# Kernel optimization log

Measured on AMD Instinct MI355X. Metric: run time of the kernel, lower is better.

The kernel has to match this reference:

```python
import jax, jax.numpy as jnp
import numpy as np

ALPHA = 0.2  # LeakyReLU negative slope
N, H, W, T, V = 4, 24, 24, 4, 32
L, NHEADS = 2, 4  # n_heads_per_layer = (4, 4)


def _norm_adj(Bp):
    # adj = B + I, min-max normalized, then symmetric D^-1/2 normalization
    v = Bp.shape[0]
    adj = Bp + jnp.eye(v, dtype=Bp.dtype)
    adj = (adj - adj.min()) / (adj.max() - adj.min())
    d12 = 1.0 / jnp.sqrt(jnp.sum(adj, axis=1))  # diag of sqrt(inverse(D))
    return d12[:, None] * adj * d12[None, :]


def _head(x, mw, mb, a, Bp):
    # x: (N,H,W,T,V) -> h: (N,V,H,W,T)
    n, hh, ww, tt, vv = x.shape
    h = jnp.transpose(x, (0, 4, 1, 2, 3))
    # LinearMapping over the T axis (in_features == out_features == T)
    Wh = jnp.einsum('nvhwt,ts->nvhws', h, mw) + mb  # (N,V,H,W,T)
    # temporal all-pairs attention input: concat on the W axis, then the
    # same C-order reinterpretation torch .view does:
    rep_i = jnp.repeat(Wh, vv, axis=1)            # (N,V*V,H,W,T), i-major
    rep_j = jnp.tile(Wh, (1, vv, 1, 1, 1))        # (N,V*V,H,W,T), j-major
    a_in = jnp.concatenate([rep_i, rep_j], axis=3)  # (N,V*V,H,2W,T)
    a_in = a_in.reshape(n, vv, vv, tt, 2 * hh * ww)  # == torch .view
    e = jnp.einsum('nijtk,k->nijt', a_in, a)
    att = jax.nn.softmax(jax.nn.leaky_relu(e, ALPHA), axis=-1)  # softmax over T
    # diag_embed + matmul over j == elementwise scale over t, summed over j
    Whf = Wh.reshape(n, vv, hh * ww, tt)
    agg = jnp.einsum('njmt,nijt->nimt', Whf, att)  # (N,V,HW,T)
    adjn = _norm_adj(Bp)
    hp = jnp.einsum('nimt,iu->nmtu', agg, adjn)    # (N,HW,T,V)
    return jax.nn.elu(hp.reshape(n, hh, ww, tt, vv))


def setup_inputs() -> dict:
    key = jax.random.key(0)
    k0, k1, k2, k3 = jax.random.split(key, 4)
    x = jax.random.normal(k0, (N, H, W, T, V), dtype=jnp.float32)
    # per-layer, per-head parameters
    map_w = jax.random.normal(k1, (L, NHEADS, T, T), dtype=jnp.float32) * 0.5
    map_b = jax.random.normal(k2, (L, NHEADS, T), dtype=jnp.float32) * 0.02
    # a_temporal: (2*H*W,) per head, xavier-ish scale
    a_temp = jax.random.normal(k3, (L, NHEADS, 2 * H * W), dtype=jnp.float32) * 0.05
    B_param = jnp.full((L, NHEADS, V, V), 1e-6, dtype=jnp.float32)
    return {"x": x, "map_w": map_w, "map_b": map_b, "a_temp": a_temp, "B_param": B_param}


def reference(x, map_w, map_b, a_temp, B_param):
    out = x
    for l in range(map_w.shape[0]):
        xi = out
        heads = jax.vmap(lambda mw, mb, a, Bp: _head(xi, mw, mb, a, Bp))(
            map_w[l], map_b[l], a_temp[l], B_param[l])
        out = jnp.mean(heads, axis=0)
    return out
```

## Files before the change

kernel.cpp:

```cpp
#include <hip/hip_runtime.h>

#define MM 576
#define NBLK 256
#define NTHR 512

__device__ __forceinline__ float lrelu(float x) { return x > 0.f ? x : 0.2f * x; }
__device__ __forceinline__ float elu1(float x)  { return x > 0.f ? x : (__expf(x) - 1.f); }
__device__ __forceinline__ unsigned short f2bf(float f) {
    unsigned u = __float_as_uint(f);
    return (unsigned short)((u + 0x7FFFu + ((u >> 16) & 1u)) >> 16);
}

__device__ __forceinline__ void wh_e_body(int n, int t, int s, int b,
                                          const float* __restrict__ xb,
                                          float* __restrict__ red,
                                          const float* __restrict__ mw_l,
                                          const float* __restrict__ mb_l,
                                          const float* __restrict__ a_l,
                                          unsigned short* __restrict__ Whg,
                                          float* __restrict__ ep) {
    int tid = threadIdx.x;
    int sub = tid >> 5, v = tid & 31;
    int hd = sub & 3, r0 = sub >> 2;
    unsigned short* Wb = Whg + (size_t)b * 4608;
    float ei = 0.f, ej = 0.f;
    for (int r = r0; r < 9; r += 4) {
        int rr = s * 9 + r;
        int dh = rr / 24, wc = rr % 24;
        const float* ab = a_l + hd * 1152 + dh * 192 + wc * 4;
        float4 aiv = *(const float4*)ab;
        float4 ajv = *(const float4*)(ab + 96);
        float x0 = xb[r * 128 + v],      x1 = xb[r * 128 + 32 + v];
        float x2 = xb[r * 128 + 64 + v], x3 = xb[r * 128 + 96 + v];
#pragma unroll
        for (int tt = 0; tt < 4; ++tt) {
            float wh = fmaf(x0, mw_l[hd * 16 + tt],
                        fmaf(x1, mw_l[hd * 16 + 4 + tt],
                         fmaf(x2, mw_l[hd * 16 + 8 + tt],
                          fmaf(x3, mw_l[hd * 16 + 12 + tt], mb_l[hd * 4 + tt]))));
            Wb[((hd * 4 + tt) * 9 + r) * 32 + v] = f2bf(wh);
            ei = fmaf(wh, (&aiv.x)[tt], ei);
            ej = fmaf(wh, (&ajv.x)[tt], ej);
        }
    }
    red[(sub * 2 + 0) * 32 + v] = ei;
    red[(sub * 2 + 1) * 32 + v] = ej;
    __syncthreads();
    if (tid < 256) {
        int hdx = tid >> 6, whx = (tid >> 5) & 1, vx = tid & 31;
        float e = 0.f;
#pragma unroll
        for (int k = 0; k < 4; ++k)
            e += red[((hdx + 4 * k) * 2 + whx) * 32 + vx];
        ep[(((size_t)(n * 4 + t)) * 16 + s) * 256 + tid] = e;
    }
}

__global__ __launch_bounds__(NTHR) void k1(const float* __restrict__ x,
                                           const float* __restrict__ map_w,
                                           const float* __restrict__ map_b,
                                           const float* __restrict__ a_temp,
                                           unsigned short* __restrict__ Whg,
                                           float* __restrict__ ep0) {
    __shared__ float xb[1152];
    __shared__ float red[1024];
    int b = blockIdx.x, tid = threadIdx.x;
    int n = b >> 6, t = (b >> 4) & 3, s = b & 15;
    if (tid < 288)
        ((float4*)xb)[tid] =
            ((const float4*)(x + (size_t)(n * MM + t * 144 + s * 9) * 128))[tid];
    __syncthreads();
    wh_e_body(n, t, s, b, xb, red, map_w, map_b, a_temp, Whg, ep0);
}

__device__ __forceinline__ void adj_build_one(const float* __restrict__ B,
                                              float* __restrict__ adjf,
                                              float* __restrict__ d12s) {
    int lane = threadIdx.x & 63;
    int u = lane & 31;
    float val[16], lmin = 1e30f, lmax = -1e30f;
#pragma unroll
    for (int k = 0; k < 16; ++k) {
        int p = lane + 64 * k;
        float vv = B[p] + ((p >> 5) == (p & 31) ? 1.f : 0.f);
        val[k] = vv;
        lmin = fminf(lmin, vv);
        lmax = fmaxf(lmax, vv);
    }
#pragma unroll
    for (int off = 32; off; off >>= 1) {
        lmin = fminf(lmin, __shfl_xor(lmin, off, 64));
        lmax = fmaxf(lmax, __shfl_xor(lmax, off, 64));
    }
    float inv = 1.f / (lmax - lmin);
    float d12r[16];
    int h = lane >> 5;
#pragma unroll
    for (int k = 0; k < 16; ++k) {
        float r = val[k];
#pragma unroll
        for (int off = 16; off; off >>= 1) r += __shfl_xor(r, off, 64);
        float rsn = (r - 32.f * lmin) * inv;
        d12r[k] = rsqrtf(rsn);
        if (u == 2 * k + h) d12s[u] = d12r[k];
    }
#pragma unroll
    for (int k = 0; k < 16; ++k) {
        int p = lane + 64 * k;
        adjf[p] = (val[k] - lmin) * inv * d12r[k] * d12s[p & 31];
    }
}

__global__ __launch_bounds__(256) void kC(const float* __restrict__ Bp_l,
                                          const float* __restrict__ ep,
                                          float* __restrict__ CT) {
    __shared__ float e[4][2][32];
    __shared__ float adjf[1024];
    __shared__ float attT[32 * 33];
    __shared__ float d12s[32];
    int b = blockIdx.x, tid = threadIdx.x;
    int n = b >> 4, hd = (b >> 2) & 3, q = b & 3;

    {
        int qp = tid >> 6, rest = tid & 63;
        const float* src = ep + ((size_t)(n * 4 + qp) * 16) * 256 + hd * 64 + rest;
        float a = 0.f;
#pragma unroll
        for (int ss = 0; ss < 16; ++ss) a += src[ss * 256];
        e[qp][rest >> 5][rest & 31] = a;
    }
    if (tid < 64) adj_build_one(Bp_l + (size_t)hd * 1024, adjf, d12s);
    __syncthreads();

    {
        int i = tid & 31;
        float ei0 = e[0][0][i], ei1 = e[1][0][i], ei2 = e[2][0][i], ei3 = e[3][0][i];
#pragma unroll
        for (int k = 0; k < 4; ++k) {
            int j = (tid + 256 * k) >> 5;
            float eq0 = lrelu(ei0 + e[0][1][j]);
            float eq1 = lrelu(ei1 + e[1][1][j]);
            float eq2 = lrelu(ei2 + e[2][1][j]);
            float eq3 = lrelu(ei3 + e[3][1][j]);
            float mx = fmaxf(fmaxf(eq0, eq1), fmaxf(eq2, eq3));
            eq0 = __expf(eq0 - mx); eq1 = __expf(eq1 - mx);
            eq2 = __expf(eq2 - mx); eq3 = __expf(eq3 - mx);
            float invs = __builtin_amdgcn_rcpf(eq0 + eq1 + eq2 + eq3);
            float num = (q & 2) ? ((q & 1) ? eq3 : eq2) : ((q & 1) ? eq1 : eq0);
            attT[j * 33 + i] = num * invs;
        }
    }
    __syncthreads();

    {
        int u = tid >> 3, j4 = (tid & 7) * 4;
        float c0 = 0.f, c1 = 0.f, c2 = 0.f, c3 = 0.f;
#pragma unroll
        for (int i = 0; i < 32; ++i) {
            float ad = adjf[i * 32 + u];
            c0 = fmaf(attT[(j4 + 0) * 33 + i], ad, c0);
            c1 = fmaf(attT[(j4 + 1) * 33 + i], ad, c1);
            c2 = fmaf(attT[(j4 + 2) * 33 + i], ad, c2);
            c3 = fmaf(attT[(j4 + 3) * 33 + i], ad, c3);
        }
        float4 cv = make_float4(c0, c1, c2, c3);
        *(float4*)&CT[(((size_t)(n * 4 + hd) * 4 + q) * 32 + u) * 32 + j4] = cv;
    }
}

template<bool LAST>
__device__ __forceinline__ void kG_body(const float* __restrict__ CT,
                                        unsigned short* __restrict__ Whg,
                                        const float* __restrict__ mw2,
                                        const float* __restrict__ mb2,
                                        const float* __restrict__ a2,
                                        float* __restrict__ ep_out,
                                        float* __restrict__ outg) {
    __shared__ unsigned short Whh[4][4][9][32];
    __shared__ float uf[3584];
    int b = blockIdx.x, tid = threadIdx.x;
    int n = b >> 6, t = (b >> 4) & 3, s = b & 15;
    int w = tid >> 6, lane = tid & 63;
    int g = w >> 2, tout = w & 3;
    int u = lane & 31, h = lane >> 5;

    float cc0[32], cc1[32];
    const float4* ct0 = (const float4*)(CT + (((size_t)(n * 4 + 2 * g) * 4 + tout) * 32 + u) * 32);
    const float4* ct1 = (const float4*)(CT + (((size_t)(n * 4 + 2 * g + 1) * 4 + tout) * 32 + u) * 32);
#pragma unroll
    for (int k = 0; k < 8; ++k) *(float4*)&cc0[4 * k] = ct0[k];
    {
        const unsigned* src = (const unsigned*)(Whg + (size_t)b * 4608);
        unsigned* dst = (unsigned*)&Whh[0][0][0][0];
#pragma unroll
        for (int k = 0; k < 4; ++k) dst[tid + 512 * k] = src[tid + 512 * k];
        if (tid < 256) dst[tid + 2048] = src[tid + 2048];
    }
#pragma unroll
    for (int k = 0; k < 8; ++k) *(float4*)&cc1[4 * k] = ct1[k];
    __syncthreads();

    float acc[5] = {0.f, 0.f, 0.f, 0.f, 0.f};
    auto gemm_hd = [&](int hd, const float (&cc)[32]) {
#pragma unroll
        for (int k = 0; k < 5; ++k) {
            int r = h ? (k < 4 ? 5 + k : 8) : k;
            const uint4* wr = (const uint4*)&Whh[hd][tout][r][0];
            float d = 0.f;
#pragma unroll
            for (int q4 = 0; q4 < 4; ++q4) {
                uint4 pk = wr[q4];
                d = fmaf(__uint_as_float(pk.x << 16),         cc[8 * q4 + 0], d);
                d = fmaf(__uint_as_float(pk.x & 0xFFFF0000u), cc[8 * q4 + 1], d);
                d = fmaf(__uint_as_float(pk.y << 16),         cc[8 * q4 + 2], d);
                d = fmaf(__uint_as_float(pk.y & 0xFFFF0000u), cc[8 * q4 + 3], d);
                d = fmaf(__uint_as_float(pk.z << 16),         cc[8 * q4 + 4], d);
                d = fmaf(__uint_as_float(pk.z & 0xFFFF0000u), cc[8 * q4 + 5], d);
                d = fmaf(__uint_as_float(pk.w << 16),         cc[8 * q4 + 6], d);
                d = fmaf(__uint_as_float(pk.w & 0xFFFF0000u), cc[8 * q4 + 7], d);
            }
            acc[k] += elu1(d);
        }
    };
    gemm_hd(2 * g,     cc0);
    gemm_hd(2 * g + 1, cc1);

    if (g == 1) {
        float* part = uf + 2304 + tout * 320;
#pragma unroll
        for (int k = 0; k < 5; ++k)
            if (h == 0 || k < 4) part[k * 64 + lane] = acc[k];
    }
    __syncthreads();
    if (g == 0) {
        const float* part = uf + 2304 + tout * 320;
#pragma unroll
        for (int k = 0; k < 5; ++k)
            if (h == 0 || k < 4) acc[k] += part[k * 64 + lane];
        if (LAST) {
            size_t mb = (size_t)(n * MM + t * 144 + s * 9);
#pragma unroll
            for (int k = 0; k < 5; ++k) {
                if (h == 0 || k < 4) {
                    int r = h ? 5 + k : k;
                    outg[((mb + r) * 4 + tout) * 32 + u] = 0.25f * acc[k];
                }
            }
        } else {
            float* xb = uf;
#pragma unroll
            for (int k = 0; k < 5; ++k) {
                if (h == 0 || k < 4) {
                    int r = h ? 5 + k : k;
                    xb[r * 128 + tout * 32 + u] = 0.25f * acc[k];
                }
            }
        }
    }

    if (!LAST) {
        __syncthreads();
        wh_e_body(n, t, s, b, uf, uf + 1216, mw2, mb2, a2, Whg, ep_out);
    }
}

__global__ __launch_bounds__(NTHR) void kG0(const float* __restrict__ CT,
                                            unsigned short* __restrict__ Whg,
                                            const float* __restrict__ mw2,
                                            const float* __restrict__ mb2,
                                            const float* __restrict__ a2,
                                            float* __restrict__ ep1) {
    kG_body<false>(CT, Whg, mw2, mb2, a2, ep1, nullptr);
}

__global__ __launch_bounds__(NTHR) void kG1(const float* __restrict__ CT,
                                            unsigned short* __restrict__ Whg,
                                            float* __restrict__ outg) {
    kG_body<true>(CT, Whg, nullptr, nullptr, nullptr, nullptr, outg);
}

extern "C" void kernel_launch(void* const* d_in, const int* in_sizes, int n_in,
                              void* d_out, int out_size, void* d_ws, size_t ws_size,
                              hipStream_t stream) {
    const float* x      = (const float*)d_in[0];
    const float* map_w  = (const float*)d_in[1];
    const float* map_b  = (const float*)d_in[2];
    const float* a_temp = (const float*)d_in[3];
    const float* Bp     = (const float*)d_in[4];
    float* out = (float*)d_out;

    unsigned short* Whg = (unsigned short*)d_ws;
    float* ep0 = (float*)((char*)d_ws + 2359296);
    float* ep1 = ep0 + 65536;
    float* CT0 = ep1 + 65536;
    float* CT1 = CT0 + 65536;

    k1 <<<NBLK, NTHR, 0, stream>>>(x, map_w, map_b, a_temp, Whg, ep0);
    kC <<<64, 256, 0, stream>>>(Bp, ep0, CT0);
    kG0<<<NBLK, NTHR, 0, stream>>>(CT0, Whg, map_w + 64, map_b + 16,
                                   a_temp + 4608, ep1);
    kC <<<64, 256, 0, stream>>>(Bp + 4096, ep1, CT1);
    kG1<<<NBLK, NTHR, 0, stream>>>(CT1, Whg, out);
}
```

Baseline: 36.94 us.

## Recompute Wh in LDS from activations instead of storing bf16 Wh to global

The bf16 Wh tensor (16 head-time planes per block) is no longer written to global memory in the first stage and read back in the aggregation kernels. Each aggregation kernel now reloads the fp32 layer input (x, or an intermediate buffer written by kG0) and recomputes Wh directly into shared memory. This trades about 9 KB of bf16 global traffic per block for 4.6 KB of fp32 input plus the recompute FMAs and an extra barrier. It also adds an intermediate-activation store in kG0.

```diff
diff --git a/kernel.cpp b/kernel.cpp
--- a/kernel.cpp
+++ b/kernel.cpp
@@ -11,18 +11,16 @@
     return (unsigned short)((u + 0x7FFFu + ((u >> 16) & 1u)) >> 16);
 }
 
-__device__ __forceinline__ void wh_e_body(int n, int t, int s, int b,
-                                          const float* __restrict__ xb,
-                                          float* __restrict__ red,
-                                          const float* __restrict__ mw_l,
-                                          const float* __restrict__ mb_l,
-                                          const float* __restrict__ a_l,
-                                          unsigned short* __restrict__ Whg,
-                                          float* __restrict__ ep) {
+__device__ __forceinline__ void e_body(int n, int t, int s,
+                                       const float* __restrict__ xb,
+                                       float* __restrict__ red,
+                                       const float* __restrict__ mw_l,
+                                       const float* __restrict__ mb_l,
+                                       const float* __restrict__ a_l,
+                                       float* __restrict__ ep) {
     int tid = threadIdx.x;
     int sub = tid >> 5, v = tid & 31;
     int hd = sub & 3, r0 = sub >> 2;
-    unsigned short* Wb = Whg + (size_t)b * 4608;
     float ei = 0.f, ej = 0.f;
     for (int r = r0; r < 9; r += 4) {
         int rr = s * 9 + r;
@@ -38,7 +36,6 @@
                         fmaf(x1, mw_l[hd * 16 + 4 + tt],
                          fmaf(x2, mw_l[hd * 16 + 8 + tt],
                           fmaf(x3, mw_l[hd * 16 + 12 + tt], mb_l[hd * 4 + tt]))));
-            Wb[((hd * 4 + tt) * 9 + r) * 32 + v] = f2bf(wh);
             ei = fmaf(wh, (&aiv.x)[tt], ei);
             ej = fmaf(wh, (&ajv.x)[tt], ej);
         }
@@ -53,6 +50,27 @@
         for (int k = 0; k < 4; ++k)
             e += red[((hdx + 4 * k) * 2 + whx) * 32 + vx];
         ep[(((size_t)(n * 4 + t)) * 16 + s) * 256 + tid] = e;
+    }
+}
+
+__device__ __forceinline__ void wh_to_lds(int s, const float* __restrict__ xb,
+                                          const float* __restrict__ mw_l,
+                                          const float* __restrict__ mb_l,
+                                          unsigned short (*Whh)[4][9][32]) {
+    int tid = threadIdx.x;
+    int sub = tid >> 5, v = tid & 31;
+    int hd = sub & 3, r0 = sub >> 2;
+    for (int r = r0; r < 9; r += 4) {
+        float x0 = xb[r * 128 + v],      x1 = xb[r * 128 + 32 + v];
+        float x2 = xb[r * 128 + 64 + v], x3 = xb[r * 128 + 96 + v];
+#pragma unroll
+        for (int tt = 0; tt < 4; ++tt) {
+            float wh = fmaf(x0, mw_l[hd * 16 + tt],
+                        fmaf(x1, mw_l[hd * 16 + 4 + tt],
+                         fmaf(x2, mw_l[hd * 16 + 8 + tt],
+                          fmaf(x3, mw_l[hd * 16 + 12 + tt], mb_l[hd * 4 + tt]))));
+            Whh[hd][tt][r][v] = f2bf(wh);
+        }
     }
 }
 
@@ -60,17 +78,15 @@
                                            const float* __restrict__ map_w,
                                            const float* __restrict__ map_b,
                                            const float* __restrict__ a_temp,
-                                           unsigned short* __restrict__ Whg,
                                            float* __restrict__ ep0) {
     __shared__ float xb[1152];
     __shared__ float red[1024];
     int b = blockIdx.x, tid = threadIdx.x;
     int n = b >> 6, t = (b >> 4) & 3, s = b & 15;
     if (tid < 288)
-        ((float4*)xb)[tid] =
-            ((const float4*)(x + (size_t)(n * MM + t * 144 + s * 9) * 128))[tid];
-    __syncthreads();
-    wh_e_body(n, t, s, b, xb, red, map_w, map_b, a_temp, Whg, ep0);
+        ((float4*)xb)[tid] = ((const float4*)(x + (size_t)b * 1152))[tid];
+    __syncthreads();
+    e_body(n, t, s, xb, red, map_w, map_b, a_temp, ep0);
 }
 
 __device__ __forceinline__ void adj_build_one(const float* __restrict__ B,
@@ -163,17 +179,20 @@
             c2 = fmaf(attT[(j4 + 2) * 33 + i], ad, c2);
             c3 = fmaf(attT[(j4 + 3) * 33 + i], ad, c3);
         }
-        float4 cv = make_float4(c0, c1, c2, c3);
-        *(float4*)&CT[(((size_t)(n * 4 + hd) * 4 + q) * 32 + u) * 32 + j4] = cv;
+        *(float4*)&CT[(((size_t)(n * 4 + hd) * 4 + q) * 32 + (tid >> 3)) * 32 + j4] =
+            make_float4(c0, c1, c2, c3);
     }
 }
 
 template<bool LAST>
-__device__ __forceinline__ void kG_body(const float* __restrict__ CT,
-                                        unsigned short* __restrict__ Whg,
+__device__ __forceinline__ void kG_body(const float* __restrict__ src,
+                                        const float* __restrict__ CT,
+                                        const float* __restrict__ mw_l,
+                                        const float* __restrict__ mb_l,
                                         const float* __restrict__ mw2,
                                         const float* __restrict__ mb2,
                                         const float* __restrict__ a2,
+                                        float* __restrict__ interg,
                                         float* __restrict__ ep_out,
                                         float* __restrict__ outg) {
     __shared__ unsigned short Whh[4][4][9][32];
@@ -184,20 +203,17 @@
     int g = w >> 2, tout = w & 3;
     int u = lane & 31, h = lane >> 5;
 
+    if (tid < 288)
+        ((float4*)uf)[tid] = ((const float4*)(src + (size_t)b * 1152))[tid];
     float cc0[32], cc1[32];
     const float4* ct0 = (const float4*)(CT + (((size_t)(n * 4 + 2 * g) * 4 + tout) * 32 + u) * 32);
     const float4* ct1 = (const float4*)(CT + (((size_t)(n * 4 + 2 * g + 1) * 4 + tout) * 32 + u) * 32);
 #pragma unroll
     for (int k = 0; k < 8; ++k) *(float4*)&cc0[4 * k] = ct0[k];
-    {
-        const unsigned* src = (const unsigned*)(Whg + (size_t)b * 4608);
-        unsigned* dst = (unsigned*)&Whh[0][0][0][0];
-#pragma unroll
-        for (int k = 0; k < 4; ++k) dst[tid + 512 * k] = src[tid + 512 * k];
-        if (tid < 256) dst[tid + 2048] = src[tid + 2048];
-    }
 #pragma unroll
     for (int k = 0; k < 8; ++k) *(float4*)&cc1[4 * k] = ct1[k];
+    __syncthreads();
+    wh_to_lds(s, uf, mw_l, mb_l, Whh);
     __syncthreads();
 
     float acc[5] = {0.f, 0.f, 0.f, 0.f, 0.f};
@@ -247,12 +263,11 @@
                 }
             }
         } else {
-            float* xb = uf;
 #pragma unroll
             for (int k = 0; k < 5; ++k) {
                 if (h == 0 || k < 4) {
                     int r = h ? 5 + k : k;
-                    xb[r * 128 + tout * 32 + u] = 0.25f * acc[k];
+                    uf[r * 128 + tout * 32 + u] = 0.25f * acc[k];
                 }
             }
         }
@@ -260,23 +275,31 @@
 
     if (!LAST) {
         __syncthreads();
-        wh_e_body(n, t, s, b, uf, uf + 1216, mw2, mb2, a2, Whg, ep_out);
-    }
-}
-
-__global__ __launch_bounds__(NTHR) void kG0(const float* __restrict__ CT,
-                                            unsigned short* __restrict__ Whg,
+        if (tid < 288)
+            ((float4*)(interg + (size_t)b * 1152))[tid] = ((const float4*)uf)[tid];
+        e_body(n, t, s, uf, uf + 1216, mw2, mb2, a2, ep_out);
+    }
+}
+
+__global__ __launch_bounds__(NTHR) void kG0(const float* __restrict__ x,
+                                            const float* __restrict__ CT,
+                                            const float* __restrict__ mw1,
+                                            const float* __restrict__ mb1,
                                             const float* __restrict__ mw2,
                                             const float* __restrict__ mb2,
                                             const float* __restrict__ a2,
+                                            float* __restrict__ interg,
                                             float* __restrict__ ep1) {
-    kG_body<false>(CT, Whg, mw2, mb2, a2, ep1, nullptr);
-}
-
-__global__ __launch_bounds__(NTHR) void kG1(const float* __restrict__ CT,
-                                            unsigned short* __restrict__ Whg,
+    kG_body<false>(x, CT, mw1, mb1, mw2, mb2, a2, interg, ep1, nullptr);
+}
+
+__global__ __launch_bounds__(NTHR) void kG1(const float* __restrict__ interg,
+                                            const float* __restrict__ CT,
+                                            const float* __restrict__ mw2,
+                                            const float* __restrict__ mb2,
                                             float* __restrict__ outg) {
-    kG_body<true>(CT, Whg, nullptr, nullptr, nullptr, nullptr, outg);
+    kG_body<true>(interg, CT, mw2, mb2, nullptr, nullptr, nullptr,
+                  nullptr, nullptr, outg);
 }
 
 extern "C" void kernel_launch(void* const* d_in, const int* in_sizes, int n_in,
@@ -289,16 +312,17 @@
     const float* Bp     = (const float*)d_in[4];
     float* out = (float*)d_out;
 
-    unsigned short* Whg = (unsigned short*)d_ws;
-    float* ep0 = (float*)((char*)d_ws + 2359296);
-    float* ep1 = ep0 + 65536;
-    float* CT0 = ep1 + 65536;
-    float* CT1 = CT0 + 65536;
-
-    k1 <<<NBLK, NTHR, 0, stream>>>(x, map_w, map_b, a_temp, Whg, ep0);
+    float* ep0    = (float*)d_ws;
+    float* ep1    = ep0 + 65536;
+    float* CT0    = ep1 + 65536;
+    float* CT1    = CT0 + 65536;
+    float* interg = CT1 + 65536;
+
+    k1 <<<NBLK, NTHR, 0, stream>>>(x, map_w, map_b, a_temp, ep0);
     kC <<<64, 256, 0, stream>>>(Bp, ep0, CT0);
-    kG0<<<NBLK, NTHR, 0, stream>>>(CT0, Whg, map_w + 64, map_b + 16,
-                                   a_temp + 4608, ep1);
+    kG0<<<NBLK, NTHR, 0, stream>>>(x, CT0, map_w, map_b,
+                                   map_w + 64, map_b + 16, a_temp + 4608,
+                                   interg, ep1);
     kC <<<64, 256, 0, stream>>>(Bp + 4096, ep1, CT1);
-    kG1<<<NBLK, NTHR, 0, stream>>>(CT1, Whg, out);
-}
+    kG1<<<NBLK, NTHR, 0, stream>>>(interg, CT1, map_w + 64, map_b + 16, out);
+}
```

Result: slower. 38.11 us (+3.1%).
